# Optimization experiments

Hardware: AMD Instinct MI355X
Metric: run time of the kernel (lower is better)

## Reference

```python
import jax, jax.numpy as jnp
import numpy as np

B, X, Y, Z, CIN = 4, 64, 64, 64, 32
COUT = 32
MX, MY, MZ = 16, 16, 16


def setup_inputs() -> dict:
    key = jax.random.key(0)
    k1, k2, k3 = jax.random.split(key, 3)
    x = jax.random.normal(k1, (B, X, Y, Z, CIN), dtype=jnp.float32)
    # Glorot-uniform-like scale for (in, out, mx, my, mz) weights
    fan = CIN + COUT
    lim = np.sqrt(6.0 / fan).astype(np.float32)
    w_real = jax.random.uniform(k2, (CIN, COUT, MX, MY, MZ), minval=-lim, maxval=lim, dtype=jnp.float32)
    w_imag = jax.random.uniform(k3, (CIN, COUT, MX, MY, MZ), minval=-lim, maxval=lim, dtype=jnp.float32)
    return {"x": x, "w_real": w_real, "w_imag": w_imag}


def reference(x, w_real, w_imag):
    # tf.signal.fft3d transforms the innermost 3 axes of the 5D input:
    # x is [B, X, Y, Z, C] so the FFT runs over (Y, Z, C) -- faithful to source.
    x_ft = jnp.fft.fftn(x.astype(jnp.complex64), axes=(-3, -2, -1))
    x_ft = jnp.transpose(x_ft, (0, 4, 1, 2, 3))            # [B, C, X, Y, Z]
    mx, my, mz = w_real.shape[2], w_real.shape[3], w_real.shape[4]
    x_crop = x_ft[:, :, :mx, :my, :mz]                     # [B, Cin, mx, my, mz]
    w = jax.lax.complex(w_real, w_imag)                    # [Cin, Cout, mx, my, mz]
    out_ft = jnp.einsum('bixyz,ioxyz->boxyz', x_crop, w)   # [B, Cout, mx, my, mz]
    sx, sy, sz = x.shape[1], x.shape[2], x.shape[3]
    out_ft = jnp.pad(out_ft, ((0, 0), (0, 0), (0, sx - mx), (0, sy - my), (0, sz - mz)))
    out_ft = jnp.transpose(out_ft, (0, 2, 3, 4, 1))        # [B, X, Y, Z, Cout]
    x_out = jnp.fft.ifftn(out_ft, axes=(-3, -2, -1))
    return jnp.real(x_out)
```

## Files before the change

kernel.cpp:

```cpp
#include <hip/hip_runtime.h>
#include <math.h>

#define PI_F 3.14159265358979323846f


__global__ __launch_bounds__(256) void k_dft_z(const float* __restrict__ x,
                                               float2* __restrict__ T1) {
    int bid = blockIdx.x;
    int ih = bid & 1, yg = (bid >> 1) & 7, xx = (bid >> 4) & 15, b = bid >> 8;
    __shared__ float  sx[8192];
    __shared__ float2 twt[1024];
    float4* sx4 = (float4*)sx;
    const float4* src4 = (const float4*)(x + (size_t)((b * 64 + xx) * 64 + yg * 8) * 2048) + ih * 4;
    #pragma unroll
    for (int t = threadIdx.x; t < 2048; t += 256) {
        int i4 = t & 3, z = (t >> 2) & 63, y = t >> 8;
        sx4[(y * 64 + z) * 4 + i4] = src4[(size_t)y * 512 + z * 8 + i4];
    }
    const float cn = -2.0f * PI_F / 64.0f;
    for (int t = threadIdx.x; t < 1024; t += 256) {
        int z = t >> 4, kz = t & 15;
        float s, c; sincosf(cn * (float)((z * kz) & 63), &s, &c);
        twt[t] = make_float2(c, s);
    }
    __syncthreads();
    int ig = threadIdx.x & 3, kz2 = (threadIdx.x >> 2) & 7, y8 = threadIdx.x >> 5;
    float ar0[4], ai0[4], ar1[4], ai1[4];
    #pragma unroll
    for (int j = 0; j < 4; j++) { ar0[j] = ai0[j] = ar1[j] = ai1[j] = 0.f; }
    const float4* twv = (const float4*)twt;
    #pragma unroll 8
    for (int z = 0; z < 64; z++) {
        float4 va = sx4[(y8 * 64 + z) * 4 + ig];
        float4 tp = twv[z * 8 + kz2];
        float v[4] = {va.x, va.y, va.z, va.w};
        #pragma unroll
        for (int j = 0; j < 4; j++) {
            ar0[j] = fmaf(v[j], tp.x, ar0[j]);
            ai0[j] = fmaf(v[j], tp.y, ai0[j]);
            ar1[j] = fmaf(v[j], tp.z, ar1[j]);
            ai1[j] = fmaf(v[j], tp.w, ai1[j]);
        }
    }
    int y = yg * 8 + y8, kz0 = kz2 * 2, i0 = ih * 16 + ig * 4;
    float2* dst = T1 + (size_t)((b * 16 + xx) * 64 + y) * 512;
    float4* d0 = (float4*)(dst + kz0 * 32 + i0);
    d0[0] = make_float4(ar0[0], ai0[0], ar0[1], ai0[1]);
    d0[1] = make_float4(ar0[2], ai0[2], ar0[3], ai0[3]);
    float4* d1 = (float4*)(dst + (kz0 + 1) * 32 + i0);
    d1[0] = make_float4(ar1[0], ai1[0], ar1[1], ai1[1]);
    d1[1] = make_float4(ar1[2], ai1[2], ar1[3], ai1[3]);
}

__global__ __launch_bounds__(256) void k_dft_y(const float2* __restrict__ T1,
                                               float2* __restrict__ XH) {
    int bid = blockIdx.x;
    int ih = bid & 1, kzg = (bid >> 1) & 3, xx = (bid >> 3) & 15, b = bid >> 7;
    __shared__ float4 sT4[2304];
    __shared__ float2 twt[1024];
    const float4* Tg4 = (const float4*)T1;
    size_t gbase = (size_t)(b * 16 + xx) * 64 * 256;
    #pragma unroll
    for (int t = threadIdx.x; t < 2048; t += 256) {
        int i4 = t & 7, kz4 = (t >> 3) & 3, y = t >> 5;
        sT4[kz4 * 576 + y * 9 + i4] =
            Tg4[gbase + (size_t)y * 256 + (kzg * 4 + kz4) * 16 + ih * 8 + i4];
    }
    const float cn = -2.0f * PI_F / 64.0f;
    for (int t = threadIdx.x; t < 1024; t += 256) {
        int y = t >> 4, ky = t & 15;
        float s, c; sincosf(cn * (float)((y * ky) & 63), &s, &c);
        twt[t] = make_float2(c, s);
    }
    __syncthreads();
    int ig = threadIdx.x & 7, ky2 = (threadIdx.x >> 3) & 7, kz4 = threadIdx.x >> 6;
    float ar[2][2], ai[2][2];
    #pragma unroll
    for (int h = 0; h < 2; h++) { ar[h][0] = ar[h][1] = ai[h][0] = ai[h][1] = 0.f; }
    const float4* twv = (const float4*)twt;
    #pragma unroll 8
    for (int y = 0; y < 64; y++) {
        float4 a  = sT4[kz4 * 576 + y * 9 + ig];
        float4 tp = twv[y * 8 + ky2];
        float xr[2] = {a.x, a.z}, xi[2] = {a.y, a.w};
        #pragma unroll
        for (int j = 0; j < 2; j++) {
            ar[0][j] += xr[j] * tp.x - xi[j] * tp.y;
            ai[0][j] += xr[j] * tp.y + xi[j] * tp.x;
            ar[1][j] += xr[j] * tp.z - xi[j] * tp.w;
            ai[1][j] += xr[j] * tp.w + xi[j] * tp.z;
        }
    }
    int kz = kzg * 4 + kz4;
    #pragma unroll
    for (int h = 0; h < 2; h++) {
        int ky = ky2 * 2 + h;
        float2* dp = XH + (((size_t)(b * 16 + xx) * 16 + ky) * 16 + kz) * 32 + ih * 16 + ig * 2;
        *(float4*)dp = make_float4(ar[h][0], ai[h][0], ar[h][1], ai[h][1]);
    }
}

__global__ __launch_bounds__(256) void k_mid(const float2* __restrict__ XH,
                                             const float* __restrict__ wr,
                                             const float* __restrict__ wi,
                                             float2* __restrict__ G) {
    int bid = blockIdx.x;
    int ky = bid & 15, xx = bid >> 4;
    __shared__ float2 sA[4 * 528];
    __shared__ float2 sB[4 * 576];
    __shared__ float2 twt[1024];
    for (int t = threadIdx.x; t < 2048; t += 256) {
        int b = t >> 9, kz = (t >> 5) & 15, i = t & 31;
        sA[b * 528 + kz * 33 + i] =
            XH[(((size_t)(b * 16 + xx) * 16 + ky) * 16 + kz) * 32 + i];
    }
    const float cn32 = -2.0f * PI_F / 32.0f;
    for (int t = threadIdx.x; t < 1024; t += 256) {
        int m = t >> 5, k = t & 31;
        float s, c; sincosf(cn32 * (float)((m * k) & 31), &s, &c);
        twt[t] = make_float2(c, s);
    }
    __syncthreads();
    const float4* twv = (const float4*)twt;
    {
        int kz = threadIdx.x & 15, ki8 = (threadIdx.x >> 4) & 3, b = threadIdx.x >> 6;
        float xr[8], xi[8];
        #pragma unroll
        for (int j = 0; j < 8; j++) { xr[j] = xi[j] = 0.f; }
        #pragma unroll 4
        for (int i = 0; i < 32; i++) {
            float2 a = sA[b * 528 + kz * 33 + i];
            #pragma unroll
            for (int k = 0; k < 4; k++) {
                float4 tp = twv[i * 16 + ki8 * 4 + k];
                xr[2 * k]     += a.x * tp.x - a.y * tp.y;
                xi[2 * k]     += a.x * tp.y + a.y * tp.x;
                xr[2 * k + 1] += a.x * tp.z - a.y * tp.w;
                xi[2 * k + 1] += a.x * tp.w + a.y * tp.z;
            }
        }
        #pragma unroll
        for (int j = 0; j < 8; j++)
            sB[b * 576 + (ki8 * 8 + j) * 18 + kz] = make_float2(xr[j], xi[j]);
    }
    __syncthreads();
    {
        int kzg = threadIdx.x & 3, o2 = (threadIdx.x >> 2) & 15, b = threadIdx.x >> 6;
        int wbase = xx * 256 + ky * 16 + kzg * 4;
        float Fr[2][4], Fi[2][4];
        #pragma unroll
        for (int h = 0; h < 2; h++)
            #pragma unroll
            for (int q = 0; q < 4; q++) { Fr[h][q] = Fi[h][q] = 0.f; }
        const float4* sB4 = (const float4*)sB;
        #pragma unroll 4
        for (int ki = 0; ki < 32; ki++) {
            float4 a01 = sB4[b * 288 + ki * 9 + kzg * 2];
            float4 a23 = sB4[b * 288 + ki * 9 + kzg * 2 + 1];
            float xr[4] = {a01.x, a01.z, a23.x, a23.z};
            float xi[4] = {a01.y, a01.w, a23.y, a23.w};
            #pragma unroll
            for (int ol = 0; ol < 2; ol++) {
                int o = o2 * 2 + ol;
                float4 w4r = *(const float4*)(wr + (size_t)(ki * 32 + o) * 4096 + wbase);
                float4 w4i = *(const float4*)(wi + (size_t)(ki * 32 + o) * 4096 + wbase);
                float wrv[4] = {w4r.x, w4r.y, w4r.z, w4r.w};
                float wiv[4] = {w4i.x, w4i.y, w4i.z, w4i.w};
                #pragma unroll
                for (int q = 0; q < 4; q++) {
                    Fr[ol][q] += xr[q] * wrv[q] - xi[q] * wiv[q];
                    Fi[ol][q] += xr[q] * wiv[q] + xi[q] * wrv[q];
                }
            }
        }
        #pragma unroll
        for (int ol = 0; ol < 2; ol++) {
            int o = o2 * 2 + ol;
            #pragma unroll
            for (int q = 0; q < 4; q++) {
                int kz = kzg * 4 + q;
                sA[b * 528 + kz * 33 + o] = make_float2(Fr[ol][q], Fi[ol][q]);
            }
        }
    }
    __syncthreads();
    {
        int kz = threadIdx.x & 15, co8 = (threadIdx.x >> 4) & 3, b = threadIdx.x >> 6;
        float gr[8], gi[8];
        #pragma unroll
        for (int j = 0; j < 8; j++) { gr[j] = gi[j] = 0.f; }
        #pragma unroll 4
        for (int o = 0; o < 32; o++) {
            float2 f = sA[b * 528 + kz * 33 + o];
            #pragma unroll
            for (int k = 0; k < 4; k++) {
                float4 tp = twv[o * 16 + co8 * 4 + k];
                gr[2 * k]     += f.x * tp.x + f.y * tp.y;
                gi[2 * k]     += f.y * tp.x - f.x * tp.y;
                gr[2 * k + 1] += f.x * tp.z + f.y * tp.w;
                gi[2 * k + 1] += f.y * tp.z - f.x * tp.w;
            }
        }
        float2* dp = G + (((size_t)(b * 16 + xx) * 16 + ky) * 16 + kz) * 32 + co8 * 8;
        ((float4*)dp)[0] = make_float4(gr[0], gi[0], gr[1], gi[1]);
        ((float4*)dp)[1] = make_float4(gr[2], gi[2], gr[3], gi[3]);
        ((float4*)dp)[2] = make_float4(gr[4], gi[4], gr[5], gi[5]);
        ((float4*)dp)[3] = make_float4(gr[6], gi[6], gr[7], gi[7]);
    }
}

__global__ __launch_bounds__(256) void k_idft_zy(const float2* __restrict__ G,
                                                 float* __restrict__ out) {
    int bid = blockIdx.x;
    int zc = bid & 7, xx = (bid >> 3) & 63, b = bid >> 9;
    float* dstb = out + (size_t)(b * 64 + xx) * 131072;
    if (xx >= 16) {
        float4* d4 = (float4*)dstb;
        for (int t = threadIdx.x; t < 4096; t += 256) {
            int y = t >> 6, r = t & 63;
            d4[(size_t)y * 512 + zc * 64 + r] = make_float4(0.f, 0.f, 0.f, 0.f);
        }
        return;
    }
    __shared__ float2 sH[128 * 34];
    __shared__ float2 twy[1024];
    __shared__ float2 twz[8 * 17];
    const float cp = 2.0f * PI_F / 64.0f;
    for (int t = threadIdx.x; t < 1024; t += 256) {
        int ky = t >> 6, y = t & 63;
        float s, c; sincosf(cp * (float)((ky * y) & 63), &s, &c);
        twy[t] = make_float2(c, s);
    }
    if (threadIdx.x < 128) {
        int dz = threadIdx.x >> 4, kz = threadIdx.x & 15;
        int z = zc * 8 + dz;
        float s, c; sincosf(cp * (float)((kz * z) & 63), &s, &c);
        twz[dz * 17 + kz] = make_float2(c, s);
    }
    __syncthreads();
    {
        int coh = threadIdx.x & 1, dz = (threadIdx.x >> 1) & 7, ky = threadIdx.x >> 4;
        const float2* Gb = G + ((size_t)(b * 16 + xx) * 16 + ky) * 512 + coh * 16;
        float Hr[16], Hi[16];
        #pragma unroll
        for (int j = 0; j < 16; j++) { Hr[j] = Hi[j] = 0.f; }
        #pragma unroll 2
        for (int kz = 0; kz < 16; kz++) {
            float2 tz = twz[dz * 17 + kz];
            #pragma unroll
            for (int k = 0; k < 8; k++) {
                float4 g = *(const float4*)(Gb + kz * 32 + k * 2);
                Hr[2 * k]     += g.x * tz.x - g.y * tz.y;
                Hi[2 * k]     += g.x * tz.y + g.y * tz.x;
                Hr[2 * k + 1] += g.z * tz.x - g.w * tz.y;
                Hi[2 * k + 1] += g.z * tz.y + g.w * tz.x;
            }
        }
        float2* hp = sH + (ky * 8 + dz) * 34 + coh * 16;
        #pragma unroll
        for (int k = 0; k < 8; k++)
            *(float4*)(hp + k * 2) = make_float4(Hr[2 * k], Hi[2 * k], Hr[2 * k + 1], Hi[2 * k + 1]);
    }
    __syncthreads();
    {
        int cog = threadIdx.x & 3, dz = (threadIdx.x >> 2) & 7, yg = threadIdx.x >> 5;
        float acc[8][8];
        #pragma unroll
        for (int yl = 0; yl < 8; yl++)
            #pragma unroll
            for (int cl = 0; cl < 8; cl++) acc[yl][cl] = 0.f;
        const float4* twy4 = (const float4*)twy;
        const float4* sH4 = (const float4*)sH;
        for (int ky = 0; ky < 16; ky++) {
            float4 t0 = twy4[ky * 32 + yg * 4 + 0];
            float4 t1 = twy4[ky * 32 + yg * 4 + 1];
            float4 t2 = twy4[ky * 32 + yg * 4 + 2];
            float4 t3 = twy4[ky * 32 + yg * 4 + 3];
            float4 h0 = sH4[(ky * 8 + dz) * 17 + cog * 4 + 0];
            float4 h1 = sH4[(ky * 8 + dz) * 17 + cog * 4 + 1];
            float4 h2 = sH4[(ky * 8 + dz) * 17 + cog * 4 + 2];
            float4 h3 = sH4[(ky * 8 + dz) * 17 + cog * 4 + 3];
            float tc[8] = {t0.x, t0.z, t1.x, t1.z, t2.x, t2.z, t3.x, t3.z};
            float ts[8] = {t0.y, t0.w, t1.y, t1.w, t2.y, t2.w, t3.y, t3.w};
            float hr[8] = {h0.x, h0.z, h1.x, h1.z, h2.x, h2.z, h3.x, h3.z};
            float hi[8] = {h0.y, h0.w, h1.y, h1.w, h2.y, h2.w, h3.y, h3.w};
            #pragma unroll
            for (int yl = 0; yl < 8; yl++)
                #pragma unroll
                for (int cl = 0; cl < 8; cl++)
                    acc[yl][cl] += tc[yl] * hr[cl] - ts[yl] * hi[cl];
        }
        const float sc = 1.0f / 131072.0f;
        #pragma unroll
        for (int yl = 0; yl < 8; yl++) {
            int y = yg * 8 + yl;
            float4* d4 = (float4*)(dstb + ((size_t)y * 64 + zc * 8 + dz) * 32 + cog * 8);
            d4[0] = make_float4(acc[yl][0] * sc, acc[yl][1] * sc, acc[yl][2] * sc, acc[yl][3] * sc);
            d4[1] = make_float4(acc[yl][4] * sc, acc[yl][5] * sc, acc[yl][6] * sc, acc[yl][7] * sc);
        }
    }
}

extern "C" void kernel_launch(void* const* d_in, const int* in_sizes, int n_in,
                              void* d_out, int out_size, void* d_ws, size_t ws_size,
                              hipStream_t stream) {
    const float* x  = (const float*)d_in[0];
    const float* wr = (const float*)d_in[1];
    const float* wi = (const float*)d_in[2];
    float* out = (float*)d_out;
    char*  ws  = (char*)d_ws;
    float2* T1 = (float2*)ws;
    float2* XH = (float2*)(ws + (size_t)16777216);
    float2* Gb = (float2*)(ws + (size_t)16777216 + 4194304);

    k_dft_z  <<<1024, 256, 0, stream>>>(x, T1);
    k_dft_y  <<< 512, 256, 0, stream>>>(T1, XH);
    k_mid    <<< 256, 256, 0, stream>>>(XH, wr, wi, Gb);
    k_idft_zy<<<2048, 256, 0, stream>>>(Gb, out);
}
```

Baseline: 288.1 us.

## Split DFT-y, mid, and inverse kernels into more blocks with less per-thread work

Three kernels get finer work decomposition. k_dft_y now handles 2 kz per block instead of 4 and doubles its grid. k_mid is split over kz quarters, quadrupling its grid and splitting the input-channel reduction across two thread halves that are combined through shared memory. k_idft_zy splits output channels in half, doubling its grid, with early exit for the zero-fill blocks. The aim is better occupancy and latency hiding on a 256-CU GPU by raising block count and cutting register and shared-memory use. The cost is recomputing twiddle tables in more blocks and extra synchronisation in k_mid.

```diff
diff --git a/kernel.cpp b/kernel.cpp
--- a/kernel.cpp
+++ b/kernel.cpp
@@ -55,16 +55,16 @@
 __global__ __launch_bounds__(256) void k_dft_y(const float2* __restrict__ T1,
                                                float2* __restrict__ XH) {
     int bid = blockIdx.x;
-    int ih = bid & 1, kzg = (bid >> 1) & 3, xx = (bid >> 3) & 15, b = bid >> 7;
-    __shared__ float4 sT4[2304];
+    int ih = bid & 1, kzg = (bid >> 1) & 7, xx = (bid >> 4) & 15, b = bid >> 8;
+    __shared__ float4 sT4[2 * 576];
     __shared__ float2 twt[1024];
     const float4* Tg4 = (const float4*)T1;
     size_t gbase = (size_t)(b * 16 + xx) * 64 * 256;
     #pragma unroll
-    for (int t = threadIdx.x; t < 2048; t += 256) {
-        int i4 = t & 7, kz4 = (t >> 3) & 3, y = t >> 5;
-        sT4[kz4 * 576 + y * 9 + i4] =
-            Tg4[gbase + (size_t)y * 256 + (kzg * 4 + kz4) * 16 + ih * 8 + i4];
+    for (int t = threadIdx.x; t < 1024; t += 256) {
+        int i4 = t & 7, kzl = (t >> 3) & 1, y = t >> 4;
+        sT4[kzl * 576 + y * 9 + i4] =
+            Tg4[gbase + (size_t)y * 256 + (kzg * 2 + kzl) * 16 + ih * 8 + i4];
     }
     const float cn = -2.0f * PI_F / 64.0f;
     for (int t = threadIdx.x; t < 1024; t += 256) {
@@ -73,31 +73,20 @@
         twt[t] = make_float2(c, s);
     }
     __syncthreads();
-    int ig = threadIdx.x & 7, ky2 = (threadIdx.x >> 3) & 7, kz4 = threadIdx.x >> 6;
-    float ar[2][2], ai[2][2];
-    #pragma unroll
-    for (int h = 0; h < 2; h++) { ar[h][0] = ar[h][1] = ai[h][0] = ai[h][1] = 0.f; }
-    const float4* twv = (const float4*)twt;
+    int ig = threadIdx.x & 7, kzl = (threadIdx.x >> 3) & 1, ky = threadIdx.x >> 4;
+    float ar0 = 0.f, ai0 = 0.f, ar1 = 0.f, ai1 = 0.f;
     #pragma unroll 8
     for (int y = 0; y < 64; y++) {
-        float4 a  = sT4[kz4 * 576 + y * 9 + ig];
-        float4 tp = twv[y * 8 + ky2];
-        float xr[2] = {a.x, a.z}, xi[2] = {a.y, a.w};
-        #pragma unroll
-        for (int j = 0; j < 2; j++) {
-            ar[0][j] += xr[j] * tp.x - xi[j] * tp.y;
-            ai[0][j] += xr[j] * tp.y + xi[j] * tp.x;
-            ar[1][j] += xr[j] * tp.z - xi[j] * tp.w;
-            ai[1][j] += xr[j] * tp.w + xi[j] * tp.z;
-        }
-    }
-    int kz = kzg * 4 + kz4;
-    #pragma unroll
-    for (int h = 0; h < 2; h++) {
-        int ky = ky2 * 2 + h;
-        float2* dp = XH + (((size_t)(b * 16 + xx) * 16 + ky) * 16 + kz) * 32 + ih * 16 + ig * 2;
-        *(float4*)dp = make_float4(ar[h][0], ai[h][0], ar[h][1], ai[h][1]);
-    }
+        float4 a  = sT4[kzl * 576 + y * 9 + ig];
+        float2 tp = twt[y * 16 + ky];
+        ar0 += a.x * tp.x - a.y * tp.y;
+        ai0 += a.x * tp.y + a.y * tp.x;
+        ar1 += a.z * tp.x - a.w * tp.y;
+        ai1 += a.z * tp.y + a.w * tp.x;
+    }
+    int kz = kzg * 2 + kzl;
+    float2* dp = XH + (((size_t)(b * 16 + xx) * 16 + ky) * 16 + kz) * 32 + ih * 16 + ig * 2;
+    *(float4*)dp = make_float4(ar0, ai0, ar1, ai1);
 }
 
 __global__ __launch_bounds__(256) void k_mid(const float2* __restrict__ XH,
@@ -105,14 +94,14 @@
                                              const float* __restrict__ wi,
                                              float2* __restrict__ G) {
     int bid = blockIdx.x;
-    int ky = bid & 15, xx = bid >> 4;
-    __shared__ float2 sA[4 * 528];
-    __shared__ float2 sB[4 * 576];
+    int kzq = bid & 3, ky = (bid >> 2) & 15, xx = bid >> 6;
+    __shared__ float2 sA[4 * 132];
+    __shared__ float2 sB[4 * 192];
     __shared__ float2 twt[1024];
-    for (int t = threadIdx.x; t < 2048; t += 256) {
-        int b = t >> 9, kz = (t >> 5) & 15, i = t & 31;
-        sA[b * 528 + kz * 33 + i] =
-            XH[(((size_t)(b * 16 + xx) * 16 + ky) * 16 + kz) * 32 + i];
+    for (int t = threadIdx.x; t < 512; t += 256) {
+        int i = t & 31, kz = (t >> 5) & 3, b = t >> 7;
+        sA[b * 132 + kz * 33 + i] =
+            XH[(((size_t)(b * 16 + xx) * 16 + ky) * 16 + kzq * 4 + kz) * 32 + i];
     }
     const float cn32 = -2.0f * PI_F / 32.0f;
     for (int t = threadIdx.x; t < 1024; t += 256) {
@@ -123,98 +112,86 @@
     __syncthreads();
     const float4* twv = (const float4*)twt;
     {
-        int kz = threadIdx.x & 15, ki8 = (threadIdx.x >> 4) & 3, b = threadIdx.x >> 6;
-        float xr[8], xi[8];
-        #pragma unroll
-        for (int j = 0; j < 8; j++) { xr[j] = xi[j] = 0.f; }
+        int kz = threadIdx.x & 3, kig = (threadIdx.x >> 2) & 15, b = threadIdx.x >> 6;
+        float xr0 = 0.f, xi0 = 0.f, xr1 = 0.f, xi1 = 0.f;
+        #pragma unroll 8
+        for (int i = 0; i < 32; i++) {
+            float2 a  = sA[b * 132 + kz * 33 + i];
+            float4 tp = twv[i * 16 + kig];
+            xr0 += a.x * tp.x - a.y * tp.y;
+            xi0 += a.x * tp.y + a.y * tp.x;
+            xr1 += a.x * tp.z - a.y * tp.w;
+            xi1 += a.x * tp.w + a.y * tp.z;
+        }
+        sB[b * 192 + (kig * 2) * 6 + kz]     = make_float2(xr0, xi0);
+        sB[b * 192 + (kig * 2 + 1) * 6 + kz] = make_float2(xr1, xi1);
+    }
+    __syncthreads();
+    int o = threadIdx.x & 31, b2 = (threadIdx.x >> 5) & 3, kih = threadIdx.x >> 7;
+    float Fr[4], Fi[4];
+    {
+        #pragma unroll
+        for (int q = 0; q < 4; q++) { Fr[q] = Fi[q] = 0.f; }
+        const float4* sB4 = (const float4*)sB;
+        int wofs = xx * 256 + ky * 16 + kzq * 4;
         #pragma unroll 4
-        for (int i = 0; i < 32; i++) {
-            float2 a = sA[b * 528 + kz * 33 + i];
-            #pragma unroll
-            for (int k = 0; k < 4; k++) {
-                float4 tp = twv[i * 16 + ki8 * 4 + k];
-                xr[2 * k]     += a.x * tp.x - a.y * tp.y;
-                xi[2 * k]     += a.x * tp.y + a.y * tp.x;
-                xr[2 * k + 1] += a.x * tp.z - a.y * tp.w;
-                xi[2 * k + 1] += a.x * tp.w + a.y * tp.z;
+        for (int kk = 0; kk < 16; kk++) {
+            int ki = kih * 16 + kk;
+            float4 a01 = sB4[b2 * 96 + ki * 3];
+            float4 a23 = sB4[b2 * 96 + ki * 3 + 1];
+            float4 w4r = *(const float4*)(wr + (size_t)(ki * 32 + o) * 4096 + wofs);
+            float4 w4i = *(const float4*)(wi + (size_t)(ki * 32 + o) * 4096 + wofs);
+            float xr[4]  = {a01.x, a01.z, a23.x, a23.z};
+            float xi[4]  = {a01.y, a01.w, a23.y, a23.w};
+            float wrv[4] = {w4r.x, w4r.y, w4r.z, w4r.w};
+            float wiv[4] = {w4i.x, w4i.y, w4i.z, w4i.w};
+            #pragma unroll
+            for (int q = 0; q < 4; q++) {
+                Fr[q] += xr[q] * wrv[q] - xi[q] * wiv[q];
+                Fi[q] += xr[q] * wiv[q] + xi[q] * wrv[q];
             }
         }
-        #pragma unroll
-        for (int j = 0; j < 8; j++)
-            sB[b * 576 + (ki8 * 8 + j) * 18 + kz] = make_float2(xr[j], xi[j]);
-    }
-    __syncthreads();
-    {
-        int kzg = threadIdx.x & 3, o2 = (threadIdx.x >> 2) & 15, b = threadIdx.x >> 6;
-        int wbase = xx * 256 + ky * 16 + kzg * 4;
-        float Fr[2][4], Fi[2][4];
-        #pragma unroll
-        for (int h = 0; h < 2; h++)
-            #pragma unroll
-            for (int q = 0; q < 4; q++) { Fr[h][q] = Fi[h][q] = 0.f; }
-        const float4* sB4 = (const float4*)sB;
-        #pragma unroll 4
-        for (int ki = 0; ki < 32; ki++) {
-            float4 a01 = sB4[b * 288 + ki * 9 + kzg * 2];
-            float4 a23 = sB4[b * 288 + ki * 9 + kzg * 2 + 1];
-            float xr[4] = {a01.x, a01.z, a23.x, a23.z};
-            float xi[4] = {a01.y, a01.w, a23.y, a23.w};
-            #pragma unroll
-            for (int ol = 0; ol < 2; ol++) {
-                int o = o2 * 2 + ol;
-                float4 w4r = *(const float4*)(wr + (size_t)(ki * 32 + o) * 4096 + wbase);
-                float4 w4i = *(const float4*)(wi + (size_t)(ki * 32 + o) * 4096 + wbase);
-                float wrv[4] = {w4r.x, w4r.y, w4r.z, w4r.w};
-                float wiv[4] = {w4i.x, w4i.y, w4i.z, w4i.w};
-                #pragma unroll
-                for (int q = 0; q < 4; q++) {
-                    Fr[ol][q] += xr[q] * wrv[q] - xi[q] * wiv[q];
-                    Fi[ol][q] += xr[q] * wiv[q] + xi[q] * wrv[q];
-                }
-            }
-        }
-        #pragma unroll
-        for (int ol = 0; ol < 2; ol++) {
-            int o = o2 * 2 + ol;
-            #pragma unroll
-            for (int q = 0; q < 4; q++) {
-                int kz = kzg * 4 + q;
-                sA[b * 528 + kz * 33 + o] = make_float2(Fr[ol][q], Fi[ol][q]);
-            }
-        }
-    }
-    __syncthreads();
-    {
-        int kz = threadIdx.x & 15, co8 = (threadIdx.x >> 4) & 3, b = threadIdx.x >> 6;
-        float gr[8], gi[8];
-        #pragma unroll
-        for (int j = 0; j < 8; j++) { gr[j] = gi[j] = 0.f; }
-        #pragma unroll 4
-        for (int o = 0; o < 32; o++) {
-            float2 f = sA[b * 528 + kz * 33 + o];
-            #pragma unroll
-            for (int k = 0; k < 4; k++) {
-                float4 tp = twv[o * 16 + co8 * 4 + k];
-                gr[2 * k]     += f.x * tp.x + f.y * tp.y;
-                gi[2 * k]     += f.y * tp.x - f.x * tp.y;
-                gr[2 * k + 1] += f.x * tp.z + f.y * tp.w;
-                gi[2 * k + 1] += f.y * tp.z - f.x * tp.w;
-            }
-        }
-        float2* dp = G + (((size_t)(b * 16 + xx) * 16 + ky) * 16 + kz) * 32 + co8 * 8;
-        ((float4*)dp)[0] = make_float4(gr[0], gi[0], gr[1], gi[1]);
-        ((float4*)dp)[1] = make_float4(gr[2], gi[2], gr[3], gi[3]);
-        ((float4*)dp)[2] = make_float4(gr[4], gi[4], gr[5], gi[5]);
-        ((float4*)dp)[3] = make_float4(gr[6], gi[6], gr[7], gi[7]);
+    }
+    __syncthreads();
+    float2* scratch = sB;
+    if (kih == 1) {
+        #pragma unroll
+        for (int q = 0; q < 4; q++)
+            scratch[(b2 * 32 + o) * 4 + q] = make_float2(Fr[q], Fi[q]);
+    }
+    __syncthreads();
+    if (kih == 0) {
+        #pragma unroll
+        for (int q = 0; q < 4; q++) {
+            float2 p = scratch[(b2 * 32 + o) * 4 + q];
+            sA[b2 * 132 + q * 33 + o] = make_float2(Fr[q] + p.x, Fi[q] + p.y);
+        }
+    }
+    __syncthreads();
+    {
+        int kz = threadIdx.x & 3, cog = (threadIdx.x >> 2) & 15, b = threadIdx.x >> 6;
+        float gr0 = 0.f, gi0 = 0.f, gr1 = 0.f, gi1 = 0.f;
+        #pragma unroll 8
+        for (int oo = 0; oo < 32; oo++) {
+            float2 f  = sA[b * 132 + kz * 33 + oo];
+            float4 tp = twv[oo * 16 + cog];
+            gr0 += f.x * tp.x + f.y * tp.y;
+            gi0 += f.y * tp.x - f.x * tp.y;
+            gr1 += f.x * tp.z + f.y * tp.w;
+            gi1 += f.y * tp.z - f.x * tp.w;
+        }
+        float2* dp = G + (((size_t)(b * 16 + xx) * 16 + ky) * 16 + kzq * 4 + kz) * 32 + cog * 2;
+        *(float4*)dp = make_float4(gr0, gi0, gr1, gi1);
     }
 }
 
 __global__ __launch_bounds__(256) void k_idft_zy(const float2* __restrict__ G,
                                                  float* __restrict__ out) {
     int bid = blockIdx.x;
-    int zc = bid & 7, xx = (bid >> 3) & 63, b = bid >> 9;
+    int ch = bid & 1, zc = (bid >> 1) & 7, xx = (bid >> 4) & 63, b = bid >> 10;
     float* dstb = out + (size_t)(b * 64 + xx) * 131072;
     if (xx >= 16) {
+        if (ch) return;
         float4* d4 = (float4*)dstb;
         for (int t = threadIdx.x; t < 4096; t += 256) {
             int y = t >> 6, r = t & 63;
@@ -222,7 +199,7 @@
         }
         return;
     }
-    __shared__ float2 sH[128 * 34];
+    __shared__ float2 sH[128 * 18];
     __shared__ float2 twy[1024];
     __shared__ float2 twz[8 * 17];
     const float cp = 2.0f * PI_F / 64.0f;
@@ -239,16 +216,16 @@
     }
     __syncthreads();
     {
-        int coh = threadIdx.x & 1, dz = (threadIdx.x >> 1) & 7, ky = threadIdx.x >> 4;
-        const float2* Gb = G + ((size_t)(b * 16 + xx) * 16 + ky) * 512 + coh * 16;
-        float Hr[16], Hi[16];
-        #pragma unroll
-        for (int j = 0; j < 16; j++) { Hr[j] = Hi[j] = 0.f; }
-        #pragma unroll 2
+        int coq = threadIdx.x & 1, dz = (threadIdx.x >> 1) & 7, ky = threadIdx.x >> 4;
+        const float2* Gb = G + ((size_t)(b * 16 + xx) * 16 + ky) * 512 + ch * 16 + coq * 8;
+        float Hr[8], Hi[8];
+        #pragma unroll
+        for (int j = 0; j < 8; j++) { Hr[j] = Hi[j] = 0.f; }
+        #pragma unroll 4
         for (int kz = 0; kz < 16; kz++) {
             float2 tz = twz[dz * 17 + kz];
             #pragma unroll
-            for (int k = 0; k < 8; k++) {
+            for (int k = 0; k < 4; k++) {
                 float4 g = *(const float4*)(Gb + kz * 32 + k * 2);
                 Hr[2 * k]     += g.x * tz.x - g.y * tz.y;
                 Hi[2 * k]     += g.x * tz.y + g.y * tz.x;
@@ -256,45 +233,43 @@
                 Hi[2 * k + 1] += g.z * tz.y + g.w * tz.x;
             }
         }
-        float2* hp = sH + (ky * 8 + dz) * 34 + coh * 16;
-        #pragma unroll
-        for (int k = 0; k < 8; k++)
+        float2* hp = sH + (ky * 8 + dz) * 18 + coq * 8;
+        #pragma unroll
+        for (int k = 0; k < 4; k++)
             *(float4*)(hp + k * 2) = make_float4(Hr[2 * k], Hi[2 * k], Hr[2 * k + 1], Hi[2 * k + 1]);
     }
     __syncthreads();
     {
-        int cog = threadIdx.x & 3, dz = (threadIdx.x >> 2) & 7, yg = threadIdx.x >> 5;
-        float acc[8][8];
-        #pragma unroll
-        for (int yl = 0; yl < 8; yl++)
+        int cog = threadIdx.x & 1, dz = (threadIdx.x >> 1) & 7, yg = threadIdx.x >> 4;
+        float acc[4][8];
+        #pragma unroll
+        for (int yl = 0; yl < 4; yl++)
             #pragma unroll
             for (int cl = 0; cl < 8; cl++) acc[yl][cl] = 0.f;
         const float4* twy4 = (const float4*)twy;
         const float4* sH4 = (const float4*)sH;
         for (int ky = 0; ky < 16; ky++) {
-            float4 t0 = twy4[ky * 32 + yg * 4 + 0];
-            float4 t1 = twy4[ky * 32 + yg * 4 + 1];
-            float4 t2 = twy4[ky * 32 + yg * 4 + 2];
-            float4 t3 = twy4[ky * 32 + yg * 4 + 3];
-            float4 h0 = sH4[(ky * 8 + dz) * 17 + cog * 4 + 0];
-            float4 h1 = sH4[(ky * 8 + dz) * 17 + cog * 4 + 1];
-            float4 h2 = sH4[(ky * 8 + dz) * 17 + cog * 4 + 2];
-            float4 h3 = sH4[(ky * 8 + dz) * 17 + cog * 4 + 3];
-            float tc[8] = {t0.x, t0.z, t1.x, t1.z, t2.x, t2.z, t3.x, t3.z};
-            float ts[8] = {t0.y, t0.w, t1.y, t1.w, t2.y, t2.w, t3.y, t3.w};
+            float4 t0 = twy4[ky * 32 + yg * 2 + 0];
+            float4 t1 = twy4[ky * 32 + yg * 2 + 1];
+            float4 h0 = sH4[(ky * 8 + dz) * 9 + cog * 4 + 0];
+            float4 h1 = sH4[(ky * 8 + dz) * 9 + cog * 4 + 1];
+            float4 h2 = sH4[(ky * 8 + dz) * 9 + cog * 4 + 2];
+            float4 h3 = sH4[(ky * 8 + dz) * 9 + cog * 4 + 3];
+            float tc[4] = {t0.x, t0.z, t1.x, t1.z};
+            float ts[4] = {t0.y, t0.w, t1.y, t1.w};
             float hr[8] = {h0.x, h0.z, h1.x, h1.z, h2.x, h2.z, h3.x, h3.z};
             float hi[8] = {h0.y, h0.w, h1.y, h1.w, h2.y, h2.w, h3.y, h3.w};
             #pragma unroll
-            for (int yl = 0; yl < 8; yl++)
+            for (int yl = 0; yl < 4; yl++)
                 #pragma unroll
                 for (int cl = 0; cl < 8; cl++)
                     acc[yl][cl] += tc[yl] * hr[cl] - ts[yl] * hi[cl];
         }
         const float sc = 1.0f / 131072.0f;
         #pragma unroll
-        for (int yl = 0; yl < 8; yl++) {
-            int y = yg * 8 + yl;
-            float4* d4 = (float4*)(dstb + ((size_t)y * 64 + zc * 8 + dz) * 32 + cog * 8);
+        for (int yl = 0; yl < 4; yl++) {
+            int y = yg * 4 + yl;
+            float4* d4 = (float4*)(dstb + ((size_t)y * 64 + zc * 8 + dz) * 32 + ch * 16 + cog * 8);
             d4[0] = make_float4(acc[yl][0] * sc, acc[yl][1] * sc, acc[yl][2] * sc, acc[yl][3] * sc);
             d4[1] = make_float4(acc[yl][4] * sc, acc[yl][5] * sc, acc[yl][6] * sc, acc[yl][7] * sc);
         }
@@ -314,7 +289,7 @@
     float2* Gb = (float2*)(ws + (size_t)16777216 + 4194304);
 
     k_dft_z  <<<1024, 256, 0, stream>>>(x, T1);
-    k_dft_y  <<< 512, 256, 0, stream>>>(T1, XH);
-    k_mid    <<< 256, 256, 0, stream>>>(XH, wr, wi, Gb);
-    k_idft_zy<<<2048, 256, 0, stream>>>(Gb, out);
-}
+    k_dft_y  <<<1024, 256, 0, stream>>>(T1, XH);
+    k_mid    <<<1024, 256, 0, stream>>>(XH, wr, wi, Gb);
+    k_idft_zy<<<4096, 256, 0, stream>>>(Gb, out);
+}
```

Result: slower. 322.2 us (+11.8%).

## Move zero-fill of output tail into first kernel and split idft blocks by channel half

Applied to the files above, without the earlier changes.

The zeroing of output rows xx>=16 moves out of the final inverse-DFT kernel and into extra blocks appended to the first forward-DFT kernel, so it overlaps with the compute blocks there. The inverse kernel now launches only for the 16 live x slices and splits the 32 output channels into two halves per block, which halves per-thread accumulators and shared memory and should improve occupancy. A __syncthreads is also added in k_mid before its shared-memory writes. The cost is extra blocks in the first kernel and recomputed twiddles in the inverse kernel across twice as many compute blocks.

```diff
diff --git a/kernel.cpp b/kernel.cpp
--- a/kernel.cpp
+++ b/kernel.cpp
@@ -5,8 +5,18 @@
 
 
 __global__ __launch_bounds__(256) void k_dft_z(const float* __restrict__ x,
-                                               float2* __restrict__ T1) {
+                                               float2* __restrict__ T1,
+                                               float* __restrict__ out) {
     int bid = blockIdx.x;
+    if (bid >= 1024) {
+        int f = bid - 1024;
+        int b = f / 384, rem = f - b * 384;
+        float4* d4 = (float4*)(out + (size_t)(b * 64 + 16) * 131072) + (size_t)rem * 4096;
+        #pragma unroll
+        for (int r = 0; r < 16; ++r)
+            d4[r * 256 + threadIdx.x] = make_float4(0.f, 0.f, 0.f, 0.f);
+        return;
+    }
     int ih = bid & 1, yg = (bid >> 1) & 7, xx = (bid >> 4) & 15, b = bid >> 8;
     __shared__ float  sx[8192];
     __shared__ float2 twt[1024];
@@ -173,6 +183,7 @@
                 }
             }
         }
+        __syncthreads();
         #pragma unroll
         for (int ol = 0; ol < 2; ol++) {
             int o = o2 * 2 + ol;
@@ -212,17 +223,9 @@
 __global__ __launch_bounds__(256) void k_idft_zy(const float2* __restrict__ G,
                                                  float* __restrict__ out) {
     int bid = blockIdx.x;
-    int zc = bid & 7, xx = (bid >> 3) & 63, b = bid >> 9;
+    int ch = bid & 1, zc = (bid >> 1) & 7, xx = (bid >> 4) & 15, b = bid >> 8;
     float* dstb = out + (size_t)(b * 64 + xx) * 131072;
-    if (xx >= 16) {
-        float4* d4 = (float4*)dstb;
-        for (int t = threadIdx.x; t < 4096; t += 256) {
-            int y = t >> 6, r = t & 63;
-            d4[(size_t)y * 512 + zc * 64 + r] = make_float4(0.f, 0.f, 0.f, 0.f);
-        }
-        return;
-    }
-    __shared__ float2 sH[128 * 34];
+    __shared__ float2 sH[128 * 18];
     __shared__ float2 twy[1024];
     __shared__ float2 twz[8 * 17];
     const float cp = 2.0f * PI_F / 64.0f;
@@ -239,16 +242,16 @@
     }
     __syncthreads();
     {
-        int coh = threadIdx.x & 1, dz = (threadIdx.x >> 1) & 7, ky = threadIdx.x >> 4;
-        const float2* Gb = G + ((size_t)(b * 16 + xx) * 16 + ky) * 512 + coh * 16;
-        float Hr[16], Hi[16];
-        #pragma unroll
-        for (int j = 0; j < 16; j++) { Hr[j] = Hi[j] = 0.f; }
-        #pragma unroll 2
+        int coq = threadIdx.x & 1, dz = (threadIdx.x >> 1) & 7, ky = threadIdx.x >> 4;
+        const float2* Gb = G + ((size_t)(b * 16 + xx) * 16 + ky) * 512 + ch * 16 + coq * 8;
+        float Hr[8], Hi[8];
+        #pragma unroll
+        for (int j = 0; j < 8; j++) { Hr[j] = Hi[j] = 0.f; }
+        #pragma unroll 4
         for (int kz = 0; kz < 16; kz++) {
             float2 tz = twz[dz * 17 + kz];
             #pragma unroll
-            for (int k = 0; k < 8; k++) {
+            for (int k = 0; k < 4; k++) {
                 float4 g = *(const float4*)(Gb + kz * 32 + k * 2);
                 Hr[2 * k]     += g.x * tz.x - g.y * tz.y;
                 Hi[2 * k]     += g.x * tz.y + g.y * tz.x;
@@ -256,45 +259,43 @@
                 Hi[2 * k + 1] += g.z * tz.y + g.w * tz.x;
             }
         }
-        float2* hp = sH + (ky * 8 + dz) * 34 + coh * 16;
-        #pragma unroll
-        for (int k = 0; k < 8; k++)
+        float2* hp = sH + (ky * 8 + dz) * 18 + coq * 8;
+        #pragma unroll
+        for (int k = 0; k < 4; k++)
             *(float4*)(hp + k * 2) = make_float4(Hr[2 * k], Hi[2 * k], Hr[2 * k + 1], Hi[2 * k + 1]);
     }
     __syncthreads();
     {
-        int cog = threadIdx.x & 3, dz = (threadIdx.x >> 2) & 7, yg = threadIdx.x >> 5;
-        float acc[8][8];
-        #pragma unroll
-        for (int yl = 0; yl < 8; yl++)
+        int cog = threadIdx.x & 1, dz = (threadIdx.x >> 1) & 7, yg = threadIdx.x >> 4;
+        float acc[4][8];
+        #pragma unroll
+        for (int yl = 0; yl < 4; yl++)
             #pragma unroll
             for (int cl = 0; cl < 8; cl++) acc[yl][cl] = 0.f;
         const float4* twy4 = (const float4*)twy;
         const float4* sH4 = (const float4*)sH;
         for (int ky = 0; ky < 16; ky++) {
-            float4 t0 = twy4[ky * 32 + yg * 4 + 0];
-            float4 t1 = twy4[ky * 32 + yg * 4 + 1];
-            float4 t2 = twy4[ky * 32 + yg * 4 + 2];
-            float4 t3 = twy4[ky * 32 + yg * 4 + 3];
-            float4 h0 = sH4[(ky * 8 + dz) * 17 + cog * 4 + 0];
-            float4 h1 = sH4[(ky * 8 + dz) * 17 + cog * 4 + 1];
-            float4 h2 = sH4[(ky * 8 + dz) * 17 + cog * 4 + 2];
-            float4 h3 = sH4[(ky * 8 + dz) * 17 + cog * 4 + 3];
-            float tc[8] = {t0.x, t0.z, t1.x, t1.z, t2.x, t2.z, t3.x, t3.z};
-            float ts[8] = {t0.y, t0.w, t1.y, t1.w, t2.y, t2.w, t3.y, t3.w};
+            float4 t0 = twy4[ky * 32 + yg * 2 + 0];
+            float4 t1 = twy4[ky * 32 + yg * 2 + 1];
+            float4 h0 = sH4[(ky * 8 + dz) * 9 + cog * 4 + 0];
+            float4 h1 = sH4[(ky * 8 + dz) * 9 + cog * 4 + 1];
+            float4 h2 = sH4[(ky * 8 + dz) * 9 + cog * 4 + 2];
+            float4 h3 = sH4[(ky * 8 + dz) * 9 + cog * 4 + 3];
+            float tc[4] = {t0.x, t0.z, t1.x, t1.z};
+            float ts[4] = {t0.y, t0.w, t1.y, t1.w};
             float hr[8] = {h0.x, h0.z, h1.x, h1.z, h2.x, h2.z, h3.x, h3.z};
             float hi[8] = {h0.y, h0.w, h1.y, h1.w, h2.y, h2.w, h3.y, h3.w};
             #pragma unroll
-            for (int yl = 0; yl < 8; yl++)
+            for (int yl = 0; yl < 4; yl++)
                 #pragma unroll
                 for (int cl = 0; cl < 8; cl++)
                     acc[yl][cl] += tc[yl] * hr[cl] - ts[yl] * hi[cl];
         }
         const float sc = 1.0f / 131072.0f;
         #pragma unroll
-        for (int yl = 0; yl < 8; yl++) {
-            int y = yg * 8 + yl;
-            float4* d4 = (float4*)(dstb + ((size_t)y * 64 + zc * 8 + dz) * 32 + cog * 8);
+        for (int yl = 0; yl < 4; yl++) {
+            int y = yg * 4 + yl;
+            float4* d4 = (float4*)(dstb + ((size_t)y * 64 + zc * 8 + dz) * 32 + ch * 16 + cog * 8);
             d4[0] = make_float4(acc[yl][0] * sc, acc[yl][1] * sc, acc[yl][2] * sc, acc[yl][3] * sc);
             d4[1] = make_float4(acc[yl][4] * sc, acc[yl][5] * sc, acc[yl][6] * sc, acc[yl][7] * sc);
         }
@@ -313,8 +314,8 @@
     float2* XH = (float2*)(ws + (size_t)16777216);
     float2* Gb = (float2*)(ws + (size_t)16777216 + 4194304);
 
-    k_dft_z  <<<1024, 256, 0, stream>>>(x, T1);
+    k_dft_z  <<<2560, 256, 0, stream>>>(x, T1, out);
     k_dft_y  <<< 512, 256, 0, stream>>>(T1, XH);
     k_mid    <<< 256, 256, 0, stream>>>(XH, wr, wi, Gb);
-    k_idft_zy<<<2048, 256, 0, stream>>>(Gb, out);
-}
+    k_idft_zy<<<1024, 256, 0, stream>>>(Gb, out);
+}
```

After: 291.0 us. No clear change (+1.0%).
